# Optimization experiments

Measured on AMD Instinct MI355X. Metric: run time of the kernel, lower is better.

The kernel has to match this reference:

```python
import jax, jax.numpy as jnp
import numpy as np


def setup_inputs() -> dict:
    key = jax.random.key(0)
    k1, k2 = jax.random.split(key)
    B, N, D = 4, 4096, 512
    q = jax.random.normal(k1, (B, N, D), dtype=jnp.float32)
    kv = jax.random.normal(k2, (B, N, D), dtype=jnp.float32)
    return {"q": q, "kv": kv}


def reference(q, kv):
    # q, kv: [B, N, D]
    scale = (kv.shape[-1] // 2) ** (-0.5)
    # full QK^T needed for the softmax row normalizer: [B, N, N]
    scores = jnp.einsum('bnd,bmd->bnm', q, kv) * scale
    lse = jax.nn.logsumexp(scores, axis=-1)          # [B, N]
    # diagonal logits computed directly (avoids re-reading the full matrix)
    diag = jnp.einsum('bnd,bnd->bn', q, kv) * scale  # [B, N]
    # masked_select with an eye mask returns the diagonal softmax entries,
    # flattened in row-major order -> shape [B*N]
    return jnp.exp(diag - lse).reshape(-1)
```

## Files before the change

kernel.cpp:

```cpp
#include <hip/hip_runtime.h>
#include <hip/hip_fp16.h>


typedef _Float16 f16x8 __attribute__((ext_vector_type(8)));
typedef float    f32x4 __attribute__((ext_vector_type(4)));

#define NB 4
#define NN 4096
#define ND 512
#define SCALE 0.0625f
#define LOG2E 1.4426950408889634f
#define NROWS (NB * NN)
#define FRAG_B 1024
#define GRP_B  16384
#define CPITCH 520

__device__ __forceinline__ void gld16(const void* g, void* l) {
    __builtin_amdgcn_global_load_lds(
        (const __attribute__((address_space(1))) unsigned int*)g,
        (__attribute__((address_space(3))) unsigned int*)l, 16, 0, 0);
}

__device__ __forceinline__ void vmfence() {
    asm volatile("s_waitcnt vmcnt(0)" ::: "memory");
}

__device__ __forceinline__ f16x8 cvt8(float4 a, float4 b) {
    f16x8 r;
    r[0] = (_Float16)a.x; r[1] = (_Float16)a.y; r[2] = (_Float16)a.z; r[3] = (_Float16)a.w;
    r[4] = (_Float16)b.x; r[5] = (_Float16)b.y; r[6] = (_Float16)b.z; r[7] = (_Float16)b.w;
    return r;
}

__device__ __forceinline__ f16x8 cvt8s(float4 a, float4 b, float s) {
    f16x8 r;
    r[0] = (_Float16)(a.x * s); r[1] = (_Float16)(a.y * s);
    r[2] = (_Float16)(a.z * s); r[3] = (_Float16)(a.w * s);
    r[4] = (_Float16)(b.x * s); r[5] = (_Float16)(b.y * s);
    r[6] = (_Float16)(b.z * s); r[7] = (_Float16)(b.w * s);
    return r;
}

__device__ __forceinline__ float sel4(const f32x4& a, int j) {
    return (j == 0) ? a[0] : (j == 1) ? a[1] : (j == 2) ? a[2] : a[3];
}

__launch_bounds__(256)
__global__ void convert_kernel(const float* __restrict__ kv,
                               _Float16* __restrict__ kvp) {
    __shared__ _Float16 s[16 * CPITCH];
    const int g    = blockIdx.x;
    const int tid  = threadIdx.x;
    const int wid  = tid >> 6;
    const int lane = tid & 63;
    const int l15  = lane & 15;
    const int quad = lane >> 4;

    #pragma unroll
    for (int i = 0; i < 4; ++i) {
        const int r = wid * 4 + i;
        const float* src = kv + ((size_t)g * 16 + r) * ND + lane * 8;
        float4 a = *(const float4*)src;
        float4 b = *(const float4*)(src + 4);
        *(f16x8*)(s + r * CPITCH + lane * 8) = cvt8(a, b);
    }
    __syncthreads();

    _Float16* dst = kvp + (size_t)g * 8192 + lane * 8;
    #pragma unroll
    for (int p = 0; p < 4; ++p) {
        const int kt = wid * 4 + p;
        f16x8 v = *(const f16x8*)(s + l15 * CPITCH + kt * 32 + quad * 8);
        *(f16x8*)(dst + kt * 512) = v;
    }
}

__launch_bounds__(128, 2)
__global__ void lse_partial_kernel(const float* __restrict__ q,
                                   const _Float16* __restrict__ kvp,
                                   float* __restrict__ partial,
                                   float* __restrict__ diagsc) {
    __shared__ char sbuf[2][GRP_B];

    const int bc = blockIdx.x;
    const int b  = bc >> 2;
    const int cs = bc & 3;
    const int rb = blockIdx.y;
    const int tid  = threadIdx.x;
    const int wid  = tid >> 6;
    const int lane = tid & 63;
    const int l15  = lane & 15;
    const int quad = lane >> 4;

    const int row0 = rb * 64 + wid * 32;
    const bool aligned = ((row0 >> 10) == cs);
    const int itd0 = aligned ? ((row0 & 1023) >> 4) : -1;
    const int itd1 = aligned ? itd0 + 1 : -1;

    f16x8 Af[2][16];
    #pragma unroll
    for (int m = 0; m < 2; ++m) {
        const float* qrow = q + ((size_t)(b * NN + row0 + m * 16 + l15)) * ND + quad * 8;
        #pragma unroll
        for (int k = 0; k < 16; ++k) {
            float4 u0 = *(const float4*)(qrow + k * 32);
            float4 u1 = *(const float4*)(qrow + k * 32 + 4);
            Af[m][k] = cvt8s(u0, u1, SCALE * LOG2E);
        }
    }

    float lacc[2][4];
    #pragma unroll
    for (int m = 0; m < 2; ++m)
        #pragma unroll
        for (int j = 0; j < 4; ++j)
            lacc[m][j] = 0.f;

    const char* pb  = (const char*)kvp + ((size_t)(b * 256 + cs * 64)) * GRP_B;
    const char* ssb = pb + (size_t)lane * 16;

    #define STAGE(it_, buf_)                                                  \
        do {                                                                  \
            const char* sp_ = ssb + (size_t)(it_) * GRP_B;                    \
            char* lb_ = sbuf[buf_];                                           \
            _Pragma("unroll")                                                 \
            for (int p_ = 0; p_ < 8; ++p_) {                                  \
                int f_ = wid * 8 + p_;                                        \
                gld16(sp_ + f_ * FRAG_B, lb_ + f_ * FRAG_B);                  \
            }                                                                 \
        } while (0)

    STAGE(0, 0);
    int buf = 0;

    for (int it = 0; it < 64; ++it) {
        vmfence();
        __syncthreads();
        if (it + 1 < 64) STAGE(it + 1, buf ^ 1);

        const char* lb = sbuf[buf] + (size_t)lane * 16;
        f32x4 acc0 = (f32x4){0.f, 0.f, 0.f, 0.f};
        f32x4 acc1 = (f32x4){0.f, 0.f, 0.f, 0.f};

        #pragma unroll
        for (int kt = 0; kt < 16; ++kt) {
            f16x8 b0 = *(const f16x8*)(lb + kt * FRAG_B);
            acc0 = __builtin_amdgcn_mfma_f32_16x16x32_f16(Af[0][kt], b0, acc0, 0, 0, 0);
            acc1 = __builtin_amdgcn_mfma_f32_16x16x32_f16(Af[1][kt], b0, acc1, 0, 0, 0);
        }

        if (it == itd0 && (l15 >> 2) == quad)
            diagsc[b * NN + row0 + l15] = sel4(acc0, l15 & 3);
        if (it == itd1 && (l15 >> 2) == quad)
            diagsc[b * NN + row0 + 16 + l15] = sel4(acc1, l15 & 3);

        #pragma unroll
        for (int j = 0; j < 4; ++j) {
            lacc[0][j] += __builtin_amdgcn_exp2f(acc0[j]);
            lacc[1][j] += __builtin_amdgcn_exp2f(acc1[j]);
        }

        buf ^= 1;
    }

    #pragma unroll
    for (int m = 0; m < 2; ++m)
        #pragma unroll
        for (int j = 0; j < 4; ++j) {
            float v = lacc[m][j];
            v += __shfl_xor(v, 1, 64);
            v += __shfl_xor(v, 2, 64);
            v += __shfl_xor(v, 4, 64);
            v += __shfl_xor(v, 8, 64);
            if (l15 == 0)
                partial[(size_t)cs * NROWS + b * NN + row0 + m * 16 + quad * 4 + j] = v;
        }
}

__launch_bounds__(256)
__global__ void finalize_kernel(const float* __restrict__ partial,
                                const float* __restrict__ diagsc,
                                float* __restrict__ out) {
    const int idx = blockIdx.x * 256 + threadIdx.x;
    float l = partial[idx] + partial[NROWS + idx] +
              partial[2 * NROWS + idx] + partial[3 * NROWS + idx];
    out[idx] = exp2f(diagsc[idx]) / l;
}

extern "C" void kernel_launch(void* const* d_in, const int* in_sizes, int n_in,
                              void* d_out, int out_size, void* d_ws, size_t ws_size,
                              hipStream_t stream) {
    const float* q  = (const float*)d_in[0];
    const float* kv = (const float*)d_in[1];
    float* out = (float*)d_out;

    _Float16* kvp   = (_Float16*)d_ws;
    float* partial  = (float*)((char*)d_ws + (size_t)NROWS * ND * 2);
    float* diagsc   = partial + 4 * NROWS;

    convert_kernel<<<1024, 256, 0, stream>>>(kv, kvp);
    lse_partial_kernel<<<dim3(16, 64), 128, 0, stream>>>(q, kvp, partial, diagsc);
    finalize_kernel<<<NROWS / 256, 256, 0, stream>>>(partial, diagsc, out);
}
```

Baseline: 174.0 us.

## Use single-wave blocks with 64 query rows per wave, dropping block barriers

The LSE kernel now runs one 64-lane wave per block instead of two. Each wave holds 64 query rows (four 16-row MFMA tiles) in registers, so every staged KV fragment from LDS feeds four MFMAs instead of two. With a single wave per block the per-iteration __syncthreads is removed, and diagonal scores are kept in registers and written once at the end. The cost is much higher register pressure (64 f16x8 A fragments plus accumulators), fewer waves in flight to hide latency, and each wave issuing all 16 global-to-LDS loads per stage on its own.

```diff
diff --git a/kernel.cpp b/kernel.cpp
--- a/kernel.cpp
+++ b/kernel.cpp
@@ -75,7 +75,7 @@
     }
 }
 
-__launch_bounds__(128, 2)
+__launch_bounds__(64, 1)
 __global__ void lse_partial_kernel(const float* __restrict__ q,
                                    const _Float16* __restrict__ kvp,
                                    float* __restrict__ partial,
@@ -86,20 +86,17 @@
     const int b  = bc >> 2;
     const int cs = bc & 3;
     const int rb = blockIdx.y;
-    const int tid  = threadIdx.x;
-    const int wid  = tid >> 6;
-    const int lane = tid & 63;
+    const int lane = threadIdx.x;
     const int l15  = lane & 15;
     const int quad = lane >> 4;
 
-    const int row0 = rb * 64 + wid * 32;
+    const int row0 = rb * 64;
     const bool aligned = ((row0 >> 10) == cs);
-    const int itd0 = aligned ? ((row0 & 1023) >> 4) : -1;
-    const int itd1 = aligned ? itd0 + 1 : -1;
-
-    f16x8 Af[2][16];
-    #pragma unroll
-    for (int m = 0; m < 2; ++m) {
+    const int itd = aligned ? ((row0 & 1023) >> 4) : -100;
+
+    f16x8 Af[4][16];
+    #pragma unroll
+    for (int m = 0; m < 4; ++m) {
         const float* qrow = q + ((size_t)(b * NN + row0 + m * 16 + l15)) * ND + quad * 8;
         #pragma unroll
         for (int k = 0; k < 16; ++k) {
@@ -109,12 +106,14 @@
         }
     }
 
-    float lacc[2][4];
-    #pragma unroll
-    for (int m = 0; m < 2; ++m)
+    float lacc[4][4];
+    #pragma unroll
+    for (int m = 0; m < 4; ++m)
         #pragma unroll
         for (int j = 0; j < 4; ++j)
             lacc[m][j] = 0.f;
+
+    float dsave[4] = {0.f, 0.f, 0.f, 0.f};
 
     const char* pb  = (const char*)kvp + ((size_t)(b * 256 + cs * 64)) * GRP_B;
     const char* ssb = pb + (size_t)lane * 16;
@@ -124,10 +123,8 @@
             const char* sp_ = ssb + (size_t)(it_) * GRP_B;                    \
             char* lb_ = sbuf[buf_];                                           \
             _Pragma("unroll")                                                 \
-            for (int p_ = 0; p_ < 8; ++p_) {                                  \
-                int f_ = wid * 8 + p_;                                        \
-                gld16(sp_ + f_ * FRAG_B, lb_ + f_ * FRAG_B);                  \
-            }                                                                 \
+            for (int p_ = 0; p_ < 16; ++p_)                                   \
+                gld16(sp_ + p_ * FRAG_B, lb_ + p_ * FRAG_B);                  \
         } while (0)
 
     STAGE(0, 0);
@@ -135,36 +132,44 @@
 
     for (int it = 0; it < 64; ++it) {
         vmfence();
-        __syncthreads();
         if (it + 1 < 64) STAGE(it + 1, buf ^ 1);
 
         const char* lb = sbuf[buf] + (size_t)lane * 16;
-        f32x4 acc0 = (f32x4){0.f, 0.f, 0.f, 0.f};
-        f32x4 acc1 = (f32x4){0.f, 0.f, 0.f, 0.f};
+        f32x4 acc[4];
+        #pragma unroll
+        for (int m = 0; m < 4; ++m)
+            acc[m] = (f32x4){0.f, 0.f, 0.f, 0.f};
 
         #pragma unroll
         for (int kt = 0; kt < 16; ++kt) {
             f16x8 b0 = *(const f16x8*)(lb + kt * FRAG_B);
-            acc0 = __builtin_amdgcn_mfma_f32_16x16x32_f16(Af[0][kt], b0, acc0, 0, 0, 0);
-            acc1 = __builtin_amdgcn_mfma_f32_16x16x32_f16(Af[1][kt], b0, acc1, 0, 0, 0);
+            #pragma unroll
+            for (int m = 0; m < 4; ++m)
+                acc[m] = __builtin_amdgcn_mfma_f32_16x16x32_f16(Af[m][kt], b0, acc[m], 0, 0, 0);
         }
 
-        if (it == itd0 && (l15 >> 2) == quad)
-            diagsc[b * NN + row0 + l15] = sel4(acc0, l15 & 3);
-        if (it == itd1 && (l15 >> 2) == quad)
-            diagsc[b * NN + row0 + 16 + l15] = sel4(acc1, l15 & 3);
-
-        #pragma unroll
-        for (int j = 0; j < 4; ++j) {
-            lacc[0][j] += __builtin_amdgcn_exp2f(acc0[j]);
-            lacc[1][j] += __builtin_amdgcn_exp2f(acc1[j]);
-        }
+        if (it == itd)     dsave[0] = sel4(acc[0], l15 & 3);
+        if (it == itd + 1) dsave[1] = sel4(acc[1], l15 & 3);
+        if (it == itd + 2) dsave[2] = sel4(acc[2], l15 & 3);
+        if (it == itd + 3) dsave[3] = sel4(acc[3], l15 & 3);
+
+        #pragma unroll
+        for (int m = 0; m < 4; ++m)
+            #pragma unroll
+            for (int j = 0; j < 4; ++j)
+                lacc[m][j] += __builtin_amdgcn_exp2f(acc[m][j]);
 
         buf ^= 1;
     }
 
-    #pragma unroll
-    for (int m = 0; m < 2; ++m)
+    if (aligned && (l15 >> 2) == quad) {
+        #pragma unroll
+        for (int m = 0; m < 4; ++m)
+            diagsc[b * NN + row0 + m * 16 + l15] = dsave[m];
+    }
+
+    #pragma unroll
+    for (int m = 0; m < 4; ++m)
         #pragma unroll
         for (int j = 0; j < 4; ++j) {
             float v = lacc[m][j];
@@ -199,6 +204,6 @@
     float* diagsc   = partial + 4 * NROWS;
 
     convert_kernel<<<1024, 256, 0, stream>>>(kv, kvp);
-    lse_partial_kernel<<<dim3(16, 64), 128, 0, stream>>>(q, kvp, partial, diagsc);
+    lse_partial_kernel<<<dim3(16, 64), 64, 0, stream>>>(q, kvp, partial, diagsc);
     finalize_kernel<<<NROWS / 256, 256, 0, stream>>>(partial, diagsc, out);
 }
```

Measured after the change: 185.8 us. 6.8% more time.
